# Performance work log

Measured on AMD Instinct MI355X. Metric: run time of the kernel, lower is better.

Reference implementation:

```python
import jax, jax.numpy as jnp
import numpy as np

H = 4        # no_heads
CH = 32      # per-head hidden (c_hidden)
INF = 1.0e9

def setup_inputs() -> dict:
    key = jax.random.key(0)
    ks = jax.random.split(key, 8)
    B, I, J, C = 1, 256, 256, 128
    s = 0.02
    return {
        "x": jax.random.normal(ks[0], (B, I, J, C), jnp.float32),
        "mask": jnp.ones((B, I, J), jnp.float32),
        "chunk_size": 0,
        "ln_w": jnp.ones((C,), jnp.float32),
        "ln_b": jnp.zeros((C,), jnp.float32),
        "w_tri": jax.random.normal(ks[1], (C, H), jnp.float32) * s,
        "wq": jax.random.normal(ks[2], (C, H * CH), jnp.float32) * s,
        "wk": jax.random.normal(ks[3], (C, H * CH), jnp.float32) * s,
        "wv": jax.random.normal(ks[4], (C, H * CH), jnp.float32) * s,
        "wg": jax.random.normal(ks[5], (C, H * CH), jnp.float32) * s,
        "bg": jnp.zeros((H * CH,), jnp.float32),
        "wo": jax.random.normal(ks[6], (H * CH, C), jnp.float32) * s,
        "bo": jnp.zeros((C,), jnp.float32),
    }

def _layer_norm(x, w, b, eps=1e-5):
    mu = jnp.mean(x, axis=-1, keepdims=True)
    var = jnp.mean(jnp.square(x - mu), axis=-1, keepdims=True)
    return (x - mu) * jax.lax.rsqrt(var + eps) * w + b

def reference(x, mask, chunk_size, ln_w, ln_b, w_tri, wq, wk, wv, wg, bg, wo, bo):
    # starting=True -> no transpose of (I, J)
    B, I, J, C = x.shape
    xn = _layer_norm(x, ln_w, ln_b)                                   # [B,I,J,C]
    # biases
    mask_bias = (INF * (mask - 1.0))[:, :, None, None, :]             # [B,I,1,1,J]
    tri_bias = jnp.einsum("bijc,ch->bhij", xn, w_tri)[:, None]        # [B,1,H,I,J]
    # gated multi-head attention over the J axis (per row I)
    q = (xn @ wq).reshape(B, I, J, H, CH) * (CH ** -0.5)              # [B,I,J,H,CH]
    k = (xn @ wk).reshape(B, I, J, H, CH)
    v = (xn @ wv).reshape(B, I, J, H, CH)
    scores = jnp.einsum("biqhd,bikhd->bihqk", q, k) + mask_bias + tri_bias
    a = jax.nn.softmax(scores, axis=-1)                               # [B,I,H,J,J]
    o = jnp.einsum("bihqk,bikhd->biqhd", a, v)                        # [B,I,J,H,CH]
    g = jax.nn.sigmoid(xn @ wg + bg).reshape(B, I, J, H, CH)
    o = (o * g).reshape(B, I, J, H * CH)
    return o @ wo + bo                                                # [B,I,J,C]
```

## Files before the change

kernel.cpp:

```cpp
#include <hip/hip_runtime.h>
#include <math.h>

#define NI 256
#define NJ 256
#define NC 128
#define NH 4
#define NCH 32

typedef __attribute__((ext_vector_type(8)))  __bf16        bf16x8;
typedef __attribute__((ext_vector_type(8)))  unsigned short u16x8;
typedef __attribute__((ext_vector_type(4)))  unsigned int   u32x4;
typedef __attribute__((ext_vector_type(16))) float         f32x16;

__device__ __forceinline__ unsigned short f2bf(float f) {
    unsigned u = __builtin_bit_cast(unsigned, f);
    u += 0x7fffu + ((u >> 16) & 1u);
    return (unsigned short)(u >> 16);
}
__device__ __forceinline__ float bf2f(unsigned short s) {
    return __builtin_bit_cast(float, ((unsigned)s) << 16);
}
__device__ __forceinline__ f32x16 fzero16() {
    f32x16 z;
#pragma unroll
    for (int r = 0; r < 16; ++r) z[r] = 0.f;
    return z;
}
__device__ __forceinline__ f32x16 mfma16(bf16x8 a, bf16x8 b, f32x16 c) {
    return __builtin_amdgcn_mfma_f32_32x32x16_bf16(a, b, c, 0, 0, 0);
}

__global__ __launch_bounds__(256) void convert_weights(
    const float* __restrict__ wq, const float* __restrict__ wk,
    const float* __restrict__ wv, const float* __restrict__ wg,
    const float* __restrict__ wo, const float* __restrict__ w_tri,
    unsigned short* __restrict__ Wt_all, unsigned short* __restrict__ Wto,
    unsigned short* __restrict__ Wtri_pad)
{
    int id = blockIdx.x * 256 + threadIdx.x;
    if (id < 4 * 16384) {
        int m = id >> 14, r = id & 16383;
        int kk = r >> 7, c = r & 127;
        const float* W = (m == 0) ? wq : (m == 1) ? wk : (m == 2) ? wv : wg;
        Wt_all[(m * 128 + c) * 128 + kk] = f2bf(W[kk * 128 + c]);
    } else if (id < 5 * 16384) {
        int r = id - 4 * 16384;
        int kk = r >> 7, c = r & 127;
        Wto[c * 128 + kk] = f2bf(wo[kk * 128 + c]);
    } else {
        int r = id - 5 * 16384;
        int col = r >> 7, kk = r & 127;
        Wtri_pad[col * 128 + kk] = (col < NH) ? f2bf(w_tri[kk * NH + col]) : (unsigned short)0;
    }
}

#define XNP 136
__global__ __launch_bounds__(256, 2) void ln_proj_mfma(
    const float* __restrict__ x, const float* __restrict__ ln_w, const float* __restrict__ ln_b,
    const unsigned short* __restrict__ Wt_all, const unsigned short* __restrict__ Wtri_pad,
    const float* __restrict__ bg,
    unsigned short* __restrict__ q, unsigned short* __restrict__ k,
    unsigned short* __restrict__ v, unsigned short* __restrict__ g,
    float* __restrict__ tri)
{
    __shared__ unsigned short xn[64 * XNP];
    const int tid = threadIdx.x;
    const long tok0 = (long)blockIdx.x * 64;

    const int lane8 = tid & 7;
#pragma unroll
    for (int p = 0; p < 2; ++p) {
        const int t = p * 32 + (tid >> 3);
        const float4* xrow = (const float4*)(x + (tok0 + t) * NC + lane8 * 16);
        float4 xv[4];
        float s = 0.f;
#pragma unroll
        for (int u = 0; u < 4; ++u) {
            xv[u] = xrow[u];
            s += xv[u].x + xv[u].y + xv[u].z + xv[u].w;
        }
#pragma unroll
        for (int off = 4; off; off >>= 1) s += __shfl_down(s, off, 8);
        const float mu = __shfl(s, 0, 8) * (1.f / (float)NC);
        float s2 = 0.f;
#pragma unroll
        for (int u = 0; u < 4; ++u) {
            float dx;
            dx = xv[u].x - mu; s2 += dx * dx;
            dx = xv[u].y - mu; s2 += dx * dx;
            dx = xv[u].z - mu; s2 += dx * dx;
            dx = xv[u].w - mu; s2 += dx * dx;
        }
#pragma unroll
        for (int off = 4; off; off >>= 1) s2 += __shfl_down(s2, off, 8);
        const float rstd = rsqrtf(__shfl(s2, 0, 8) * (1.f / (float)NC) + 1e-5f);
#pragma unroll
        for (int u = 0; u < 4; ++u) {
            const int c = lane8 * 16 + u * 4;
            const float4 lw = *(const float4*)(ln_w + c);
            const float4 lb = *(const float4*)(ln_b + c);
            float o0 = (xv[u].x - mu) * rstd * lw.x + lb.x;
            float o1 = (xv[u].y - mu) * rstd * lw.y + lb.y;
            float o2 = (xv[u].z - mu) * rstd * lw.z + lb.z;
            float o3 = (xv[u].w - mu) * rstd * lw.w + lb.w;
            unsigned p0 = (unsigned)f2bf(o0) | ((unsigned)f2bf(o1) << 16);
            unsigned p1 = (unsigned)f2bf(o2) | ((unsigned)f2bf(o3) << 16);
            *(unsigned*)&xn[t * XNP + c]     = p0;
            *(unsigned*)&xn[t * XNP + c + 2] = p1;
        }
    }
    __syncthreads();

    const int w = tid >> 6, L = tid & 63, lh = L >> 5, lc = L & 31;
    f32x16 acc[2][4], accT[2];
#pragma unroll
    for (int mt = 0; mt < 2; ++mt) {
        accT[mt] = fzero16();
#pragma unroll
        for (int nt = 0; nt < 4; ++nt) acc[mt][nt] = fzero16();
    }

#pragma unroll
    for (int k0 = 0; k0 < 8; ++k0) {
        bf16x8 a0 = *(const bf16x8*)&xn[(lc)      * XNP + k0 * 16 + lh * 8];
        bf16x8 a1 = *(const bf16x8*)&xn[(32 + lc) * XNP + k0 * 16 + lh * 8];
#pragma unroll
        for (int nt = 0; nt < 4; ++nt) {
            const int ntile = w + 4 * nt;
            bf16x8 b = *(const bf16x8*)&Wt_all[(ntile * 32 + lc) * 128 + k0 * 16 + lh * 8];
            acc[0][nt] = mfma16(a0, b, acc[0][nt]);
            acc[1][nt] = mfma16(a1, b, acc[1][nt]);
        }
        bf16x8 bt = *(const bf16x8*)&Wtri_pad[lc * 128 + k0 * 16 + lh * 8];
        accT[0] = mfma16(a0, bt, accT[0]);
        accT[1] = mfma16(a1, bt, accT[1]);
    }

    const int a_row = (int)(tok0 >> 8);
    const int b0    = (int)(tok0 & 255);
    int rowl[16];
#pragma unroll
    for (int r = 0; r < 16; ++r) rowl[r] = (r & 3) + 8 * (r >> 2) + 4 * lh;

    const float bgv = bg[w * 32 + lc];
#pragma unroll
    for (int nt = 0; nt < 4; ++nt) {
        unsigned short* O = (nt == 0) ? q : (nt == 1) ? k : (nt == 2) ? v : g;
        unsigned short* Ob = O + (((long)a_row * NH + w) * NJ + b0) * NCH + lc;
#pragma unroll
        for (int mt = 0; mt < 2; ++mt) {
#pragma unroll
            for (int r = 0; r < 16; ++r) {
                const int row = mt * 32 + rowl[r];
                float val = acc[mt][nt][r];
                if (nt == 0) val *= 0.17677669529663689f;
                if (nt == 3) val = __builtin_amdgcn_rcpf(1.f + __expf(-(val + bgv)));
                Ob[(long)row * NCH] = f2bf(val);
            }
        }
    }
    if (lc < NH) {
        float* tb = tri + ((long)lc * NI + a_row) * NJ + b0;
#pragma unroll
        for (int mt = 0; mt < 2; ++mt)
#pragma unroll
            for (int r = 0; r < 16; ++r)
                tb[mt * 32 + rowl[r]] = accT[mt][r];
    }
}

#define KSP 40
#define VTP 264
__global__ __launch_bounds__(256, 3) void attn_mfma(
    const unsigned short* __restrict__ q, const unsigned short* __restrict__ k,
    const unsigned short* __restrict__ v, const unsigned short* __restrict__ g,
    const float* __restrict__ tri, const float* __restrict__ mask,
    unsigned short* __restrict__ og)
{
    __shared__ unsigned short Ks[256 * KSP];
    __shared__ unsigned short Vt[32 * VTP];
    __shared__ float maskb[256];
    const int i = blockIdx.x, h = blockIdx.y, qh = blockIdx.z;
    const int tid = threadIdx.x;
    const int w = tid >> 6, L = tid & 63, lh = L >> 5, lc = L & 31;
    const long base = ((long)i * NH + h) * NJ * NCH;

#pragma unroll
    for (int it = 0; it < 4; ++it) {
        const int idx = it * 256 + tid;
        const int key = idx >> 2, c8 = (idx & 3) * 8;
        *(bf16x8*)&Ks[key * KSP + c8] = *(const bf16x8*)(k + base + key * NCH + c8);
    }
    {
        const int key = tid;
        const u16x8 r0 = *(const u16x8*)(v + base + key * NCH);
        const u16x8 r1 = *(const u16x8*)(v + base + key * NCH + 8);
        const u16x8 r2 = *(const u16x8*)(v + base + key * NCH + 16);
        const u16x8 r3 = *(const u16x8*)(v + base + key * NCH + 24);
#pragma unroll
        for (int u = 0; u < 8; ++u) {
            Vt[(u)      * VTP + key] = r0[u];
            Vt[(u + 8)  * VTP + key] = r1[u];
            Vt[(u + 16) * VTP + key] = r2[u];
            Vt[(u + 24) * VTP + key] = r3[u];
        }
    }
    maskb[tid] = 1.0e9f * (mask[i * NJ + tid] - 1.0f);
    __syncthreads();

    const int qt = qh * 4 + w;
    const int qbase = qt * 32;
    const int qrow  = qbase + lc;

    const bf16x8 a0 = *(const bf16x8*)(q + base + (long)qrow * NCH + lh * 8);
    const bf16x8 a1 = *(const bf16x8*)(q + base + (long)qrow * NCH + 16 + lh * 8);
    const float* trirow = tri + ((long)h * NI + qrow) * NJ;

    float ls = 0.f;
    f32x16 O = fzero16();

#pragma unroll
    for (int t = 0; t < 8; ++t) {
        bf16x8 kb0 = *(const bf16x8*)&Ks[(t * 32 + lc) * KSP + lh * 8];
        bf16x8 kb1 = *(const bf16x8*)&Ks[(t * 32 + lc) * KSP + 16 + lh * 8];
        f32x16 s = fzero16();
        s = mfma16(kb0, a0, s);
        s = mfma16(kb1, a1, s);

        unsigned pk[8];
#pragma unroll
        for (int gg = 0; gg < 4; ++gg) {
            const int kb = t * 32 + gg * 8 + 4 * lh;
            const float4 tb = *(const float4*)(trirow + kb);
            const float4 mb = *(const float4*)&maskb[kb];
            const float p0 = __expf(fminf(s[4 * gg + 0] + tb.x + mb.x, 30.f));
            const float p1 = __expf(fminf(s[4 * gg + 1] + tb.y + mb.y, 30.f));
            const float p2 = __expf(fminf(s[4 * gg + 2] + tb.z + mb.z, 30.f));
            const float p3 = __expf(fminf(s[4 * gg + 3] + tb.w + mb.w, 30.f));
            ls += (p0 + p1) + (p2 + p3);
            pk[2 * gg]     = (unsigned)f2bf(p0) | ((unsigned)f2bf(p1) << 16);
            pk[2 * gg + 1] = (unsigned)f2bf(p2) | ((unsigned)f2bf(p3) << 16);
        }

#pragma unroll
        for (int ss = 0; ss < 2; ++ss) {
            const unsigned give0 = lh ? pk[4 * ss]     : pk[4 * ss + 2];
            const unsigned give1 = lh ? pk[4 * ss + 1] : pk[4 * ss + 3];
            const unsigned t0 = __shfl_xor(give0, 32);
            const unsigned t1 = __shfl_xor(give1, 32);
            u32x4 bw;
            bw[0] = lh ? t0 : pk[4 * ss];
            bw[1] = lh ? t1 : pk[4 * ss + 1];
            bw[2] = lh ? pk[4 * ss + 2] : t0;
            bw[3] = lh ? pk[4 * ss + 3] : t1;
            const bf16x8 pb = __builtin_bit_cast(bf16x8, bw);
            const bf16x8 va = *(const bf16x8*)&Vt[lc * VTP + t * 32 + ss * 16 + lh * 8];
            O = mfma16(va, pb, O);
        }
    }

    ls += __shfl_xor(ls, 32);
    const float rl = __builtin_amdgcn_rcpf(ls);
    const unsigned short* gb = g + base + (long)qrow * NCH;
    unsigned short* ob = og + ((long)i * NJ + qrow) * NC + h * NCH;
#pragma unroll
    for (int gg = 0; gg < 4; ++gg) {
        const int ch = gg * 8 + 4 * lh;
        const ushort4 gv = *(const ushort4*)(gb + ch);
        const float v0 = O[4 * gg + 0] * rl * bf2f(gv.x);
        const float v1 = O[4 * gg + 1] * rl * bf2f(gv.y);
        const float v2 = O[4 * gg + 2] * rl * bf2f(gv.z);
        const float v3 = O[4 * gg + 3] * rl * bf2f(gv.w);
        uint2 st;
        st.x = (unsigned)f2bf(v0) | ((unsigned)f2bf(v1) << 16);
        st.y = (unsigned)f2bf(v2) | ((unsigned)f2bf(v3) << 16);
        *(uint2*)(ob + ch) = st;
    }
}

#define OGP 136
__global__ __launch_bounds__(256, 4) void out_proj_mfma(
    const unsigned short* __restrict__ og, const unsigned short* __restrict__ Wto,
    const float* __restrict__ bo, float* __restrict__ out)
{
    __shared__ unsigned short t_og[64 * OGP];
    const int tid = threadIdx.x;
    const long tok0 = (long)blockIdx.x * 64;
#pragma unroll
    for (int it = 0; it < 4; ++it) {
        const int idx = it * 256 + tid;
        const int tk = idx >> 4, c8 = (idx & 15) * 8;
        *(bf16x8*)&t_og[tk * OGP + c8] = *(const bf16x8*)(og + (tok0 + tk) * NC + c8);
    }
    __syncthreads();

    const int w = tid >> 6, L = tid & 63, lh = L >> 5, lc = L & 31;
    f32x16 acc[2];
    acc[0] = fzero16(); acc[1] = fzero16();
#pragma unroll
    for (int k0 = 0; k0 < 8; ++k0) {
        bf16x8 a0 = *(const bf16x8*)&t_og[(lc)      * OGP + k0 * 16 + lh * 8];
        bf16x8 a1 = *(const bf16x8*)&t_og[(32 + lc) * OGP + k0 * 16 + lh * 8];
        bf16x8 b  = *(const bf16x8*)&Wto[(w * 32 + lc) * 128 + k0 * 16 + lh * 8];
        acc[0] = mfma16(a0, b, acc[0]);
        acc[1] = mfma16(a1, b, acc[1]);
    }
    const float bov = bo[w * 32 + lc];
#pragma unroll
    for (int mt = 0; mt < 2; ++mt)
#pragma unroll
        for (int r = 0; r < 16; ++r) {
            const int row = mt * 32 + (r & 3) + 8 * (r >> 2) + 4 * lh;
            out[(tok0 + row) * NC + w * 32 + lc] = acc[mt][r] + bov;
        }
}

extern "C" void kernel_launch(void* const* d_in, const int* in_sizes, int n_in,
                              void* d_out, int out_size, void* d_ws, size_t ws_size,
                              hipStream_t stream) {
    const float* x     = (const float*)d_in[0];
    const float* mask  = (const float*)d_in[1];
    const float* ln_w  = (const float*)d_in[3];
    const float* ln_b  = (const float*)d_in[4];
    const float* w_tri = (const float*)d_in[5];
    const float* wq    = (const float*)d_in[6];
    const float* wk    = (const float*)d_in[7];
    const float* wv    = (const float*)d_in[8];
    const float* wg    = (const float*)d_in[9];
    const float* bg    = (const float*)d_in[10];
    const float* wo    = (const float*)d_in[11];
    const float* bo    = (const float*)d_in[12];
    float* out = (float*)d_out;

    char* p = (char*)d_ws;
    const long TOK = (long)NI * NJ;
    const long QB  = TOK * NC * sizeof(unsigned short);
    unsigned short* q  = (unsigned short*)p; p += QB;
    unsigned short* k  = (unsigned short*)p; p += QB;
    unsigned short* v  = (unsigned short*)p; p += QB;
    unsigned short* g  = (unsigned short*)p; p += QB;
    unsigned short* og = (unsigned short*)p; p += QB;
    float* tri = (float*)p; p += (long)NH * NI * NJ * sizeof(float);
    unsigned short* Wt_all   = (unsigned short*)p; p += 4 * 128 * 128 * sizeof(unsigned short);
    unsigned short* Wto      = (unsigned short*)p; p += 128 * 128 * sizeof(unsigned short);
    unsigned short* Wtri_pad = (unsigned short*)p; p += 32 * 128 * sizeof(unsigned short);

    hipLaunchKernelGGL(convert_weights, dim3(336), dim3(256), 0, stream,
                       wq, wk, wv, wg, wo, w_tri, Wt_all, Wto, Wtri_pad);
    hipLaunchKernelGGL(ln_proj_mfma, dim3(TOK / 64), dim3(256), 0, stream,
                       x, ln_w, ln_b, Wt_all, Wtri_pad, bg, q, k, v, g, tri);
    hipLaunchKernelGGL(attn_mfma, dim3(NI, NH, 2), dim3(256), 0, stream,
                       q, k, v, g, tri, mask, og);
    hipLaunchKernelGGL(out_proj_mfma, dim3(TOK / 64), dim3(256), 0, stream,
                       og, Wto, bo, out);
}
```

Before: 209.0 us.

## Fuse output projection into attention kernel and pre-swizzle triangle bias

Attention now loops over all four heads inside one block per row half and multiplies each head's gated output by the matching slice of the output weights, accumulating the final projection in registers. This removes the og intermediate buffer and the separate out_proj kernel. A new kernel rewrites the triangle bias into the MFMA register layout so each lane reads contiguous float4s. In exchange, the grid shrinks to 512 blocks with lower occupancy, the heads run serially inside each block, and an extra launch plus a full copy of the bias is added.

```diff
diff --git a/kernel.cpp b/kernel.cpp
--- a/kernel.cpp
+++ b/kernel.cpp
@@ -169,150 +169,205 @@
     }
 }
 
+#define LSP 260
+__global__ __launch_bounds__(256) void swizzle_triT(
+    const float* __restrict__ tri, float* __restrict__ tswz)
+{
+    __shared__ float Ls[32 * LSP];
+    const int h = blockIdx.x, qt = blockIdx.y;
+    const int tid = threadIdx.x;
+#pragma unroll
+    for (int it = 0; it < 8; ++it) {
+        const int fi = it * 256 + tid;
+        const int row = fi >> 6, c4 = fi & 63;
+        *(float4*)&Ls[row * LSP + c4 * 4] =
+            *(const float4*)(tri + ((long)h * NI + qt * 32 + row) * NJ + c4 * 4);
+    }
+    __syncthreads();
+    const int kt = tid >> 5;
+    const int lane2 = (tid & 31) * 2;
+    float* dst = tswz + (((long)(h * 8 + qt) * 8 + kt) * 64 + lane2) * 16;
+#pragma unroll
+    for (int sub = 0; sub < 2; ++sub) {
+        const int lane = lane2 + sub;
+        const int lc = lane & 31, lhh = lane >> 5;
+        float vals[16];
+#pragma unroll
+        for (int r = 0; r < 16; ++r)
+            vals[r] = Ls[lc * LSP + kt * 32 + (r & 3) + 8 * (r >> 2) + 4 * lhh];
+#pragma unroll
+        for (int u = 0; u < 4; ++u)
+            *(float4*)(dst + sub * 16 + u * 4) =
+                make_float4(vals[4*u], vals[4*u+1], vals[4*u+2], vals[4*u+3]);
+    }
+}
+
 #define KSP 40
 #define VTP 264
-__global__ __launch_bounds__(256, 3) void attn_mfma(
+#define GSP 40
+#define OSP 36
+__global__ __launch_bounds__(256, 2) void attn_fused(
     const unsigned short* __restrict__ q, const unsigned short* __restrict__ k,
     const unsigned short* __restrict__ v, const unsigned short* __restrict__ g,
-    const float* __restrict__ tri, const float* __restrict__ mask,
-    unsigned short* __restrict__ og)
+    const float* __restrict__ tswz, const float* __restrict__ mask,
+    const unsigned short* __restrict__ Wto, const float* __restrict__ bo,
+    float* __restrict__ out)
 {
-    __shared__ unsigned short Ks[256 * KSP];
-    __shared__ unsigned short Vt[32 * VTP];
-    __shared__ float maskb[256];
-    const int i = blockIdx.x, h = blockIdx.y, qh = blockIdx.z;
+    __shared__ char smem[48640];
+    unsigned short* Ks = (unsigned short*)smem;
+    unsigned short* Vt = (unsigned short*)(smem + 20480);
+    unsigned short* Gs = (unsigned short*)(smem + 37376);
+    float*       maskb = (float*)(smem + 47616);
+    float*        outs = (float*)smem;
+
+    const int i = blockIdx.x, qh = blockIdx.y;
     const int tid = threadIdx.x;
     const int w = tid >> 6, L = tid & 63, lh = L >> 5, lc = L & 31;
-    const long base = ((long)i * NH + h) * NJ * NCH;
-
-#pragma unroll
-    for (int it = 0; it < 4; ++it) {
-        const int idx = it * 256 + tid;
-        const int key = idx >> 2, c8 = (idx & 3) * 8;
-        *(bf16x8*)&Ks[key * KSP + c8] = *(const bf16x8*)(k + base + key * NCH + c8);
-    }
-    {
-        const int key = tid;
-        const u16x8 r0 = *(const u16x8*)(v + base + key * NCH);
-        const u16x8 r1 = *(const u16x8*)(v + base + key * NCH + 8);
-        const u16x8 r2 = *(const u16x8*)(v + base + key * NCH + 16);
-        const u16x8 r3 = *(const u16x8*)(v + base + key * NCH + 24);
-#pragma unroll
-        for (int u = 0; u < 8; ++u) {
-            Vt[(u)      * VTP + key] = r0[u];
-            Vt[(u + 8)  * VTP + key] = r1[u];
-            Vt[(u + 16) * VTP + key] = r2[u];
-            Vt[(u + 24) * VTP + key] = r3[u];
-        }
-    }
+    const int qt = qh * 4 + w;
+    const int qrow = qt * 32 + lc;
+
     maskb[tid] = 1.0e9f * (mask[i * NJ + tid] - 1.0f);
-    __syncthreads();
-
-    const int qt = qh * 4 + w;
-    const int qbase = qt * 32;
-    const int qrow  = qbase + lc;
-
-    const bf16x8 a0 = *(const bf16x8*)(q + base + (long)qrow * NCH + lh * 8);
-    const bf16x8 a1 = *(const bf16x8*)(q + base + (long)qrow * NCH + 16 + lh * 8);
-    const float* trirow = tri + ((long)h * NI + qrow) * NJ;
-
-    float ls = 0.f;
-    f32x16 O = fzero16();
-
-#pragma unroll
-    for (int t = 0; t < 8; ++t) {
-        bf16x8 kb0 = *(const bf16x8*)&Ks[(t * 32 + lc) * KSP + lh * 8];
-        bf16x8 kb1 = *(const bf16x8*)&Ks[(t * 32 + lc) * KSP + 16 + lh * 8];
-        f32x16 s = fzero16();
-        s = mfma16(kb0, a0, s);
-        s = mfma16(kb1, a1, s);
-
-        unsigned pk[8];
+
+    f32x16 outacc[4];
+#pragma unroll
+    for (int ct = 0; ct < 4; ++ct) outacc[ct] = fzero16();
+
+    for (int h = 0; h < NH; ++h) {
+        if (h) __syncthreads();
+        const long base = ((long)i * NH + h) * NJ * NCH;
+
+#pragma unroll
+        for (int it = 0; it < 4; ++it) {
+            const int idx = it * 256 + tid;
+            const int key = idx >> 2, c8 = (idx & 3) * 8;
+            *(bf16x8*)&Ks[key * KSP + c8] = *(const bf16x8*)(k + base + key * NCH + c8);
+        }
+        {
+            const int key = tid;
+            const u16x8 r0 = *(const u16x8*)(v + base + key * NCH);
+            const u16x8 r1 = *(const u16x8*)(v + base + key * NCH + 8);
+            const u16x8 r2 = *(const u16x8*)(v + base + key * NCH + 16);
+            const u16x8 r3 = *(const u16x8*)(v + base + key * NCH + 24);
+#pragma unroll
+            for (int u = 0; u < 8; ++u) {
+                Vt[(u)      * VTP + key] = r0[u];
+                Vt[(u + 8)  * VTP + key] = r1[u];
+                Vt[(u + 16) * VTP + key] = r2[u];
+                Vt[(u + 24) * VTP + key] = r3[u];
+            }
+        }
+#pragma unroll
+        for (int it = 0; it < 2; ++it) {
+            const int idx = it * 256 + tid;
+            const int row = idx >> 2, c8 = (idx & 3) * 8;
+            *(bf16x8*)&Gs[row * GSP + c8] =
+                *(const bf16x8*)(g + base + (qh * 128 + row) * NCH + c8);
+        }
+        __syncthreads();
+
+        const bf16x8 a0 = *(const bf16x8*)(q + base + (long)qrow * NCH + lh * 8);
+        const bf16x8 a1 = *(const bf16x8*)(q + base + (long)qrow * NCH + 16 + lh * 8);
+        const float* tbase = tswz + ((long)(h * 8 + qt) * 8) * 1024 + (long)L * 16;
+
+        float ls = 0.f;
+        f32x16 O = fzero16();
+
+#pragma unroll
+        for (int t = 0; t < 8; ++t) {
+            bf16x8 kb0 = *(const bf16x8*)&Ks[(t * 32 + lc) * KSP + lh * 8];
+            bf16x8 kb1 = *(const bf16x8*)&Ks[(t * 32 + lc) * KSP + 16 + lh * 8];
+            f32x16 s = fzero16();
+            s = mfma16(kb0, a0, s);
+            s = mfma16(kb1, a1, s);
+
+            unsigned pk[8];
+            const float* tv = tbase + (long)t * 1024;
+#pragma unroll
+            for (int gg = 0; gg < 4; ++gg) {
+                const float4 tb = *(const float4*)(tv + gg * 4);
+                const float4 mb = *(const float4*)&maskb[t * 32 + gg * 8 + 4 * lh];
+                const float p0 = __expf(fminf(s[4 * gg + 0] + tb.x + mb.x, 30.f));
+                const float p1 = __expf(fminf(s[4 * gg + 1] + tb.y + mb.y, 30.f));
+                const float p2 = __expf(fminf(s[4 * gg + 2] + tb.z + mb.z, 30.f));
+                const float p3 = __expf(fminf(s[4 * gg + 3] + tb.w + mb.w, 30.f));
+                ls += (p0 + p1) + (p2 + p3);
+                pk[2 * gg]     = (unsigned)f2bf(p0) | ((unsigned)f2bf(p1) << 16);
+                pk[2 * gg + 1] = (unsigned)f2bf(p2) | ((unsigned)f2bf(p3) << 16);
+            }
+
+#pragma unroll
+            for (int ss = 0; ss < 2; ++ss) {
+                const unsigned give0 = lh ? pk[4 * ss]     : pk[4 * ss + 2];
+                const unsigned give1 = lh ? pk[4 * ss + 1] : pk[4 * ss + 3];
+                const unsigned t0 = __shfl_xor(give0, 32);
+                const unsigned t1 = __shfl_xor(give1, 32);
+                u32x4 bw;
+                bw[0] = lh ? t0 : pk[4 * ss];
+                bw[1] = lh ? t1 : pk[4 * ss + 1];
+                bw[2] = lh ? pk[4 * ss + 2] : t0;
+                bw[3] = lh ? pk[4 * ss + 3] : t1;
+                const bf16x8 pb = __builtin_bit_cast(bf16x8, bw);
+                const bf16x8 va = *(const bf16x8*)&Vt[lc * VTP + t * 32 + ss * 16 + lh * 8];
+                O = mfma16(va, pb, O);
+            }
+        }
+
+        ls += __shfl_xor(ls, 32);
+        const float rl = __builtin_amdgcn_rcpf(ls);
+        unsigned pk2[8];
 #pragma unroll
         for (int gg = 0; gg < 4; ++gg) {
-            const int kb = t * 32 + gg * 8 + 4 * lh;
-            const float4 tb = *(const float4*)(trirow + kb);
-            const float4 mb = *(const float4*)&maskb[kb];
-            const float p0 = __expf(fminf(s[4 * gg + 0] + tb.x + mb.x, 30.f));
-            const float p1 = __expf(fminf(s[4 * gg + 1] + tb.y + mb.y, 30.f));
-            const float p2 = __expf(fminf(s[4 * gg + 2] + tb.z + mb.z, 30.f));
-            const float p3 = __expf(fminf(s[4 * gg + 3] + tb.w + mb.w, 30.f));
-            ls += (p0 + p1) + (p2 + p3);
-            pk[2 * gg]     = (unsigned)f2bf(p0) | ((unsigned)f2bf(p1) << 16);
-            pk[2 * gg + 1] = (unsigned)f2bf(p2) | ((unsigned)f2bf(p3) << 16);
+            const ushort4 gv = *(const ushort4*)&Gs[(w * 32 + lc) * GSP + gg * 8 + 4 * lh];
+            const float o0 = O[4 * gg + 0] * rl * bf2f(gv.x);
+            const float o1 = O[4 * gg + 1] * rl * bf2f(gv.y);
+            const float o2 = O[4 * gg + 2] * rl * bf2f(gv.z);
+            const float o3 = O[4 * gg + 3] * rl * bf2f(gv.w);
+            pk2[2 * gg]     = (unsigned)f2bf(o0) | ((unsigned)f2bf(o1) << 16);
+            pk2[2 * gg + 1] = (unsigned)f2bf(o2) | ((unsigned)f2bf(o3) << 16);
         }
 
 #pragma unroll
         for (int ss = 0; ss < 2; ++ss) {
-            const unsigned give0 = lh ? pk[4 * ss]     : pk[4 * ss + 2];
-            const unsigned give1 = lh ? pk[4 * ss + 1] : pk[4 * ss + 3];
+            const unsigned give0 = lh ? pk2[4 * ss]     : pk2[4 * ss + 2];
+            const unsigned give1 = lh ? pk2[4 * ss + 1] : pk2[4 * ss + 3];
             const unsigned t0 = __shfl_xor(give0, 32);
             const unsigned t1 = __shfl_xor(give1, 32);
             u32x4 bw;
-            bw[0] = lh ? t0 : pk[4 * ss];
-            bw[1] = lh ? t1 : pk[4 * ss + 1];
-            bw[2] = lh ? pk[4 * ss + 2] : t0;
-            bw[3] = lh ? pk[4 * ss + 3] : t1;
-            const bf16x8 pb = __builtin_bit_cast(bf16x8, bw);
-            const bf16x8 va = *(const bf16x8*)&Vt[lc * VTP + t * 32 + ss * 16 + lh * 8];
-            O = mfma16(va, pb, O);
-        }
-    }
-
-    ls += __shfl_xor(ls, 32);
-    const float rl = __builtin_amdgcn_rcpf(ls);
-    const unsigned short* gb = g + base + (long)qrow * NCH;
-    unsigned short* ob = og + ((long)i * NJ + qrow) * NC + h * NCH;
-#pragma unroll
-    for (int gg = 0; gg < 4; ++gg) {
-        const int ch = gg * 8 + 4 * lh;
-        const ushort4 gv = *(const ushort4*)(gb + ch);
-        const float v0 = O[4 * gg + 0] * rl * bf2f(gv.x);
-        const float v1 = O[4 * gg + 1] * rl * bf2f(gv.y);
-        const float v2 = O[4 * gg + 2] * rl * bf2f(gv.z);
-        const float v3 = O[4 * gg + 3] * rl * bf2f(gv.w);
-        uint2 st;
-        st.x = (unsigned)f2bf(v0) | ((unsigned)f2bf(v1) << 16);
-        st.y = (unsigned)f2bf(v2) | ((unsigned)f2bf(v3) << 16);
-        *(uint2*)(ob + ch) = st;
-    }
-}
-
-#define OGP 136
-__global__ __launch_bounds__(256, 4) void out_proj_mfma(
-    const unsigned short* __restrict__ og, const unsigned short* __restrict__ Wto,
-    const float* __restrict__ bo, float* __restrict__ out)
-{
-    __shared__ unsigned short t_og[64 * OGP];
-    const int tid = threadIdx.x;
-    const long tok0 = (long)blockIdx.x * 64;
-#pragma unroll
-    for (int it = 0; it < 4; ++it) {
-        const int idx = it * 256 + tid;
-        const int tk = idx >> 4, c8 = (idx & 15) * 8;
-        *(bf16x8*)&t_og[tk * OGP + c8] = *(const bf16x8*)(og + (tok0 + tk) * NC + c8);
-    }
-    __syncthreads();
-
-    const int w = tid >> 6, L = tid & 63, lh = L >> 5, lc = L & 31;
-    f32x16 acc[2];
-    acc[0] = fzero16(); acc[1] = fzero16();
-#pragma unroll
-    for (int k0 = 0; k0 < 8; ++k0) {
-        bf16x8 a0 = *(const bf16x8*)&t_og[(lc)      * OGP + k0 * 16 + lh * 8];
-        bf16x8 a1 = *(const bf16x8*)&t_og[(32 + lc) * OGP + k0 * 16 + lh * 8];
-        bf16x8 b  = *(const bf16x8*)&Wto[(w * 32 + lc) * 128 + k0 * 16 + lh * 8];
-        acc[0] = mfma16(a0, b, acc[0]);
-        acc[1] = mfma16(a1, b, acc[1]);
-    }
-    const float bov = bo[w * 32 + lc];
-#pragma unroll
-    for (int mt = 0; mt < 2; ++mt)
-#pragma unroll
-        for (int r = 0; r < 16; ++r) {
-            const int row = mt * 32 + (r & 3) + 8 * (r >> 2) + 4 * lh;
-            out[(tok0 + row) * NC + w * 32 + lc] = acc[mt][r] + bov;
-        }
+            bw[0] = lh ? t0 : pk2[4 * ss];
+            bw[1] = lh ? t1 : pk2[4 * ss + 1];
+            bw[2] = lh ? pk2[4 * ss + 2] : t0;
+            bw[3] = lh ? pk2[4 * ss + 3] : t1;
+            const bf16x8 ogb = __builtin_bit_cast(bf16x8, bw);
+#pragma unroll
+            for (int ct = 0; ct < 4; ++ct) {
+                const bf16x8 wa = *(const bf16x8*)&Wto[(ct * 32 + lc) * 128 + h * 32 + ss * 16 + lh * 8];
+                outacc[ct] = mfma16(wa, ogb, outacc[ct]);
+            }
+        }
+    }
+
+    int rowl[16];
+#pragma unroll
+    for (int r = 0; r < 16; ++r) rowl[r] = (r & 3) + 8 * (r >> 2) + 4 * lh;
+#pragma unroll
+    for (int ct = 0; ct < 4; ++ct) {
+        __syncthreads();
+#pragma unroll
+        for (int r = 0; r < 16; ++r)
+            outs[(w * 32 + lc) * OSP + rowl[r]] = outacc[ct][r];
+        __syncthreads();
+#pragma unroll
+        for (int it = 0; it < 4; ++it) {
+            const int fi = it * 256 + tid;
+            const int row = fi >> 3, c4 = fi & 7;
+            const float4 vv = *(const float4*)&outs[row * OSP + c4 * 4];
+            const float4 bo4 = *(const float4*)(bo + ct * 32 + c4 * 4);
+            float4 st;
+            st.x = vv.x + bo4.x; st.y = vv.y + bo4.y;
+            st.z = vv.z + bo4.z; st.w = vv.w + bo4.w;
+            *(float4*)(out + ((long)i * NJ + qh * 128 + row) * NC + ct * 32 + c4 * 4) = st;
+        }
+    }
 }
 
 extern "C" void kernel_launch(void* const* d_in, const int* in_sizes, int n_in,
@@ -339,8 +394,8 @@
     unsigned short* k  = (unsigned short*)p; p += QB;
     unsigned short* v  = (unsigned short*)p; p += QB;
     unsigned short* g  = (unsigned short*)p; p += QB;
-    unsigned short* og = (unsigned short*)p; p += QB;
-    float* tri = (float*)p; p += (long)NH * NI * NJ * sizeof(float);
+    float* tri  = (float*)p; p += (long)NH * NI * NJ * sizeof(float);
+    float* tswz = (float*)p; p += (long)NH * NI * NJ * sizeof(float);
     unsigned short* Wt_all   = (unsigned short*)p; p += 4 * 128 * 128 * sizeof(unsigned short);
     unsigned short* Wto      = (unsigned short*)p; p += 128 * 128 * sizeof(unsigned short);
     unsigned short* Wtri_pad = (unsigned short*)p; p += 32 * 128 * sizeof(unsigned short);
@@ -349,8 +404,7 @@
                        wq, wk, wv, wg, wo, w_tri, Wt_all, Wto, Wtri_pad);
     hipLaunchKernelGGL(ln_proj_mfma, dim3(TOK / 64), dim3(256), 0, stream,
                        x, ln_w, ln_b, Wt_all, Wtri_pad, bg, q, k, v, g, tri);
-    hipLaunchKernelGGL(attn_mfma, dim3(NI, NH, 2), dim3(256), 0, stream,
-                       q, k, v, g, tri, mask, og);
-    hipLaunchKernelGGL(out_proj_mfma, dim3(TOK / 64), dim3(256), 0, stream,
-                       og, Wto, bo, out);
-}
+    hipLaunchKernelGGL(swizzle_triT, dim3(NH, 8), dim3(256), 0, stream, tri, tswz);
+    hipLaunchKernelGGL(attn_fused, dim3(NI, 2), dim3(256), 0, stream,
+                       q, k, v, g, tswz, mask, Wto, bo, out);
+}
```

New measurement: 179.8 us. 14.0% less time.
